# Kernel tuning notes

Hardware: AMD Instinct MI355X
Metric: run time of the kernel (lower is better)

The kernel has to match this reference:

```python
import jax, jax.numpy as jnp
import numpy as np


def setup_inputs() -> dict:
    key = jax.random.key(0)
    k1, k2 = jax.random.split(key)
    x = jax.random.normal(k1, (8, 64, 224, 224), dtype=jnp.float32)
    kernel = jax.random.normal(k2, (64, 1, 3, 3), dtype=jnp.float32)
    return {"x": x, "kernel": kernel, "stride": 1, "padding": 1, "dilation": 1}


def reference(x, kernel, stride, padding, dilation):
    # Tropical-max (morphological dilation) conv: out[b,c,i,j] =
    #   max_{ki,kj} x_pad[b,c,i*stride+ki*dilation, j*stride+kj*dilation] + kernel[c,0,ki,kj]
    # Padding uses the tropical neutral element -inf, matching the torch module.
    B, C, H, W = x.shape
    O, _, K, _ = kernel.shape
    out_h = (H + 2 * padding - dilation * (K - 1) - 1) // stride + 1
    out_w = (W + 2 * padding - dilation * (K - 1) - 1) // stride + 1
    neutral = -jnp.inf
    xp = jnp.pad(x, ((0, 0), (0, 0), (padding, padding), (padding, padding)),
                 constant_values=neutral)
    # Initialize at -inf: equivalent to the module's extra neutral pad on the K axis.
    acc = jnp.full((B, C, out_h, out_w), neutral, dtype=x.dtype)
    h_span = (out_h - 1) * stride + 1
    w_span = (out_w - 1) * stride + 1
    # Small fixed K*K loop over kernel taps; avoids materializing the unfolded tensor.
    for ki in range(K):
        for kj in range(K):
            patch = jax.lax.slice(
                xp,
                (0, 0, ki * dilation, kj * dilation),
                (B, C, ki * dilation + h_span, kj * dilation + w_span),
                (1, 1, stride, stride),
            )  # [B, C, out_h, out_w]
            acc = jnp.maximum(acc, patch + kernel[None, :, 0, ki, kj, None, None])
    return acc
```

## Files before the change

### kernel.cpp

```cpp
#include <hip/hip_runtime.h>
#include <math.h>


#define H_DIM 224
#define W_DIM 224
#define W4    56
#define ROWS  8
#define GR    28
#define C_DIM 64
#define NXCD  8

__global__ __launch_bounds__(256) void tropical_conv_kernel(
    const float* __restrict__ x,
    const float* __restrict__ kern,
    float* __restrict__ out,
    int total)
{
    int bid  = blockIdx.x;
    int cpx  = gridDim.x >> 3;
    int swz  = (bid & (NXCD - 1)) * cpx + (bid >> 3);
    int idx  = swz * blockDim.x + threadIdx.x;
    if (idx >= total) return;

    const float NEG = -INFINITY;

    int j4 = idx % W4;
    int t  = idx / W4;
    int g  = t % GR;
    int bc = t / GR;
    int c  = bc & (C_DIM - 1);

    const float* kc = kern + c * 9;
    float k00 = kc[0], k01 = kc[1], k02 = kc[2];
    float k10 = kc[3], k11 = kc[4], k12 = kc[5];
    float k20 = kc[6], k21 = kc[7], k22 = kc[8];

    const float* plane  = x   + (size_t)bc * (H_DIM * W_DIM);
    float*       oplane = out + (size_t)bc * (H_DIM * W_DIM);
    int j0 = j4 * 4;
    int i0 = g * ROWS;

    float4 rv[ROWS + 2];
    float  lf[ROWS + 2], rg[ROWS + 2];
    #pragma unroll
    for (int rr = 0; rr < ROWS + 2; ++rr) {
        int r = i0 - 1 + rr;
        if (r >= 0 && r < H_DIM) {
            const float* row = plane + r * W_DIM;
            rv[rr] = *(const float4*)(row + j0);
            lf[rr] = (j4 > 0)      ? row[j0 - 1] : NEG;
            rg[rr] = (j4 < W4 - 1) ? row[j0 + 4] : NEG;
        } else {
            rv[rr] = make_float4(NEG, NEG, NEG, NEG);
            lf[rr] = NEG;
            rg[rr] = NEG;
        }
    }

    #pragma unroll
    for (int o = 0; o < ROWS; ++o) {
        float4 acc = make_float4(NEG, NEG, NEG, NEG);
        #pragma unroll
        for (int ki = 0; ki < 3; ++ki) {
            int rr = o + ki;
            float t0 = (ki == 0) ? k00 : (ki == 1) ? k10 : k20;
            float t1 = (ki == 0) ? k01 : (ki == 1) ? k11 : k21;
            float t2 = (ki == 0) ? k02 : (ki == 1) ? k12 : k22;
            float4 a = rv[rr];
            acc.x = fmaxf(acc.x, fmaxf(fmaxf(lf[rr] + t0, a.x + t1), a.y    + t2));
            acc.y = fmaxf(acc.y, fmaxf(fmaxf(a.x    + t0, a.y + t1), a.z    + t2));
            acc.z = fmaxf(acc.z, fmaxf(fmaxf(a.y    + t0, a.z + t1), a.w    + t2));
            acc.w = fmaxf(acc.w, fmaxf(fmaxf(a.z    + t0, a.w + t1), rg[rr] + t2));
        }
        *(float4*)(oplane + (size_t)(i0 + o) * W_DIM + j0) = acc;
    }
}

extern "C" void kernel_launch(void* const* d_in, const int* in_sizes, int n_in,
                              void* d_out, int out_size, void* d_ws, size_t ws_size,
                              hipStream_t stream) {
    const float* x    = (const float*)d_in[0];
    const float* kern = (const float*)d_in[1];
    float* out        = (float*)d_out;

    const int total = 8 * C_DIM * GR * W4;
    const int block = 256;
    const int grid  = (total + block - 1) / block;
    tropical_conv_kernel<<<grid, block, 0, stream>>>(x, kern, out, total);
}
```

Baseline: 188.7 us.

## Map one wavefront per row strip and get halo columns via lane shuffles

Each 64-lane wavefront now handles a 4-row strip across the full image width, with 56 lanes doing work. Left and right halo values come from neighbouring lanes through shuffles instead of extra scalar global loads. Boundary rows use clamped loads plus masking instead of branches. This removes the redundant scalar halo loads and the divergent boundary branches, but it raises vertical halo re-reads, since the strip is 4 rows instead of 8, and leaves 8 lanes idle.

```diff
diff --git a/kernel.cpp b/kernel.cpp
--- a/kernel.cpp
+++ b/kernel.cpp
@@ -4,30 +4,25 @@
 
 #define H_DIM 224
 #define W_DIM 224
-#define W4    56
-#define ROWS  8
-#define GR    28
+#define SR    4
+#define SPP   56
 #define C_DIM 64
 #define NXCD  8
 
 __global__ __launch_bounds__(256) void tropical_conv_kernel(
     const float* __restrict__ x,
     const float* __restrict__ kern,
-    float* __restrict__ out,
-    int total)
+    float* __restrict__ out)
 {
     int bid  = blockIdx.x;
     int cpx  = gridDim.x >> 3;
     int swz  = (bid & (NXCD - 1)) * cpx + (bid >> 3);
-    int idx  = swz * blockDim.x + threadIdx.x;
-    if (idx >= total) return;
 
-    const float NEG = -INFINITY;
+    int lane = threadIdx.x & 63;
+    int wid  = swz * 4 + (threadIdx.x >> 6);
 
-    int j4 = idx % W4;
-    int t  = idx / W4;
-    int g  = t % GR;
-    int bc = t / GR;
+    int s  = wid % SPP;
+    int bc = wid / SPP;
     int c  = bc & (C_DIM - 1);
 
     const float* kc = kern + c * 9;
@@ -35,30 +30,46 @@
     float k10 = kc[3], k11 = kc[4], k12 = kc[5];
     float k20 = kc[6], k21 = kc[7], k22 = kc[8];
 
+    const float NEG = -INFINITY;
+
     const float* plane  = x   + (size_t)bc * (H_DIM * W_DIM);
     float*       oplane = out + (size_t)bc * (H_DIM * W_DIM);
-    int j0 = j4 * 4;
-    int i0 = g * ROWS;
 
-    float4 rv[ROWS + 2];
-    float  lf[ROWS + 2], rg[ROWS + 2];
+    int i0  = s * SR;
+    int cl  = (lane < 56) ? lane : 55;
+    int col = cl * 4;
+
+    float4 rv[SR + 2];
     #pragma unroll
-    for (int rr = 0; rr < ROWS + 2; ++rr) {
-        int r = i0 - 1 + rr;
-        if (r >= 0 && r < H_DIM) {
-            const float* row = plane + r * W_DIM;
-            rv[rr] = *(const float4*)(row + j0);
-            lf[rr] = (j4 > 0)      ? row[j0 - 1] : NEG;
-            rg[rr] = (j4 < W4 - 1) ? row[j0 + 4] : NEG;
-        } else {
-            rv[rr] = make_float4(NEG, NEG, NEG, NEG);
-            lf[rr] = NEG;
-            rg[rr] = NEG;
-        }
+    for (int rr = 0; rr < SR + 2; ++rr) {
+        int r  = i0 - 1 + rr;
+        int rc = r < 0 ? 0 : (r > H_DIM - 1 ? H_DIM - 1 : r);
+        rv[rr] = *(const float4*)(plane + (size_t)rc * W_DIM + col);
+    }
+    __builtin_amdgcn_sched_barrier(0);
+
+    bool top = (s == 0);
+    bool bot = (s == SPP - 1);
+    rv[0].x = top ? NEG : rv[0].x;
+    rv[0].y = top ? NEG : rv[0].y;
+    rv[0].z = top ? NEG : rv[0].z;
+    rv[0].w = top ? NEG : rv[0].w;
+    rv[SR + 1].x = bot ? NEG : rv[SR + 1].x;
+    rv[SR + 1].y = bot ? NEG : rv[SR + 1].y;
+    rv[SR + 1].z = bot ? NEG : rv[SR + 1].z;
+    rv[SR + 1].w = bot ? NEG : rv[SR + 1].w;
+
+    float lf[SR + 2], rg[SR + 2];
+    #pragma unroll
+    for (int rr = 0; rr < SR + 2; ++rr) {
+        float up = __shfl_up(rv[rr].w, 1);
+        float dn = __shfl_down(rv[rr].x, 1);
+        lf[rr] = (lane > 0)  ? up : NEG;
+        rg[rr] = (lane < 55) ? dn : NEG;
     }
 
     #pragma unroll
-    for (int o = 0; o < ROWS; ++o) {
+    for (int o = 0; o < SR; ++o) {
         float4 acc = make_float4(NEG, NEG, NEG, NEG);
         #pragma unroll
         for (int ki = 0; ki < 3; ++ki) {
@@ -72,7 +83,9 @@
             acc.z = fmaxf(acc.z, fmaxf(fmaxf(a.y    + t0, a.z + t1), a.w    + t2));
             acc.w = fmaxf(acc.w, fmaxf(fmaxf(a.z    + t0, a.w + t1), rg[rr] + t2));
         }
-        *(float4*)(oplane + (size_t)(i0 + o) * W_DIM + j0) = acc;
+        if (lane < 56) {
+            *(float4*)(oplane + (size_t)(i0 + o) * W_DIM + col) = acc;
+        }
     }
 }
 
@@ -83,8 +96,7 @@
     const float* kern = (const float*)d_in[1];
     float* out        = (float*)d_out;
 
-    const int total = 8 * C_DIM * GR * W4;
+    const int grid  = 8 * C_DIM * SPP / 4;
     const int block = 256;
-    const int grid  = (total + block - 1) / block;
-    tropical_conv_kernel<<<grid, block, 0, stream>>>(x, kern, out, total);
+    tropical_conv_kernel<<<grid, block, 0, stream>>>(x, kern, out);
 }
```

Measured after the change: 185.9 us, median of 2. Within noise of the previous version (-1.5%).
